# Kernel optimization log

Hardware: AMD Instinct MI355X
Metric: run time of the kernel (lower is better)

## Reference

```python
import jax, jax.numpy as jnp
import numpy as np

N = 50000
E = 800000
C_IN = 128
C_OUT = 128
HID = 2 * C_OUT


def setup_inputs() -> dict:
    key = jax.random.key(0)
    k1, k2, k3, k4, k5, k6, k7, k8 = jax.random.split(key, 8)
    node_feats = jax.random.normal(k1, (N, C_IN), dtype=jnp.float32)
    edge_index = jax.random.randint(k2, (2, E), 0, N, dtype=jnp.int64)
    edge_attr = jax.random.uniform(k3, (E,), dtype=jnp.float32)
    s1 = 1.0 / np.sqrt(C_IN)
    s2 = 1.0 / np.sqrt(HID)
    W1 = jax.random.uniform(k4, (C_IN, HID), dtype=jnp.float32, minval=-s1, maxval=s1)
    b1 = jax.random.uniform(k5, (HID,), dtype=jnp.float32, minval=-s1, maxval=s1)
    W2 = jax.random.uniform(k6, (HID, C_OUT), dtype=jnp.float32, minval=-s2, maxval=s2)
    b2 = jax.random.uniform(k7, (C_OUT,), dtype=jnp.float32, minval=-s2, maxval=s2)
    return {"node_feats": node_feats, "edge_index": edge_index, "edge_attr": edge_attr,
            "W1": W1, "b1": b1, "W2": W2, "b2": b2}


def _wl_conv_continuous(x, edge_index, edge_attr):
    # PyG WLConvContinuous: mean-aggregate weighted neighbor feats, then 0.5*(x + agg)
    src, dst = edge_index[0], edge_index[1]
    msg = x[src] * edge_attr[:, None]                      # [E, C_IN]
    agg = jax.ops.segment_sum(msg, dst, num_segments=N)    # [N, C_IN]
    deg = jax.ops.segment_sum(jnp.ones((E,), x.dtype), dst, num_segments=N)
    agg = agg / jnp.maximum(deg, 1.0)[:, None]             # mean aggregation
    return 0.5 * (x + agg)


def reference(node_feats, edge_index, edge_attr, W1, b1, W2, b2):
    out = _wl_conv_continuous(node_feats, edge_index, edge_attr)
    h = jax.nn.relu(out @ W1 + b1)
    return h @ W2 + b2
```

## Files before the change

kernel.cpp:

```cpp
#include <hip/hip_runtime.h>

#define C 128
#define HID 256
#define MT 64
#define EPB 2048
#define BSH 8
#define CAP 12288
#define OUTCAP (CAP + 2048)

typedef __attribute__((ext_vector_type(8))) short bf16x8;
typedef __attribute__((ext_vector_type(4))) short s16x4;
typedef __attribute__((ext_vector_type(4))) float f32x4;

__device__ inline unsigned short f2b(float f) {
    unsigned u = __builtin_bit_cast(unsigned, f);
    unsigned r = u + 0x7fffu + ((u >> 16) & 1u);
    return (unsigned short)(r >> 16);
}


__global__ __launch_bounds__(256) void fused_pre(
    const float* __restrict__ x, const float* __restrict__ W1,
    const float* __restrict__ W2, unsigned short* __restrict__ xb,
    unsigned short* __restrict__ W1p, unsigned short* __restrict__ W2p,
    int* __restrict__ cursor, long total4, int xblocks)
{
    const int bid = blockIdx.x;
    const int t = threadIdx.x;
    if (bid < xblocks) {
        long i = (long)bid * 256 + t;
        if (i < total4) {
            float4 v = *(const float4*)(x + i * 4);
            ushort4 o;
            o.x = f2b(v.x); o.y = f2b(v.y); o.z = f2b(v.z); o.w = f2b(v.w);
            *(ushort4*)(xb + i * 4) = o;
        }
    } else {
        if (bid == xblocks) cursor[t] = 0;
        int tt = (bid - xblocks) * 256 + t;
        if (tt < C * HID) {
            {
                int j = tt & 7, l = (tt >> 3) & 63, kk = (tt >> 9) & 3, nt = tt >> 11;
                int n = nt * 16 + (l & 15);
                int k = kk * 32 + 16 * (j >> 2) + 4 * (l >> 4) + (j & 3);
                W1p[tt] = f2b(W1[k * HID + n]);
            }
            {
                int j = tt & 7, l = (tt >> 3) & 63, kk = (tt >> 9) & 7, nt = tt >> 12;
                int n = nt * 16 + (l & 15);
                int k = kk * 32 + 16 * (j >> 2) + 4 * (l >> 4) + (j & 3);
                W2p[tt] = f2b(W2[k * C + n]);
            }
        }
    }
}


__global__ __launch_bounds__(256) void bucket_scatter(
    const int* __restrict__ ei, const float* __restrict__ ea,
    int* __restrict__ cursor, uint2* __restrict__ tmp, int E, int NB)
{
    __shared__ unsigned recx[EPB];
    __shared__ float    recw[EPB];
    __shared__ unsigned char bkt[EPB];
    __shared__ int bins[256];
    const int t = threadIdx.x;
    const int base = blockIdx.x * EPB;
    const int n = min(EPB, E - base);
    bins[t] = 0;
    __syncthreads();
    for (int i = t; i < n; i += 256) {
        int src = ei[base + i];
        int dst = ei[E + base + i];
        recx[i] = (unsigned)src | ((unsigned)(dst & 255) << 24);
        recw[i] = ea[base + i];
        int b = dst >> BSH;
        bkt[i] = (unsigned char)b;
        atomicAdd(&bins[b], 1);
    }
    __syncthreads();
    int myCount = bins[t];
    __syncthreads();
    int myBase = 0;
    if (t < NB && myCount > 0) myBase = atomicAdd(&cursor[t], myCount);
    bins[t] = t * CAP + myBase;
    __syncthreads();
    for (int i = t; i < n; i += 256) {
        int b = bkt[i];
        int pos = atomicAdd(&bins[b], 1);
        tmp[pos] = uint2{recx[i], __builtin_bit_cast(unsigned, recw[i])};
    }
}


__global__ __launch_bounds__(256) void bucket_sort(
    const uint2* __restrict__ tmp, const int* __restrict__ cursor,
    uint2* __restrict__ src_w, int* __restrict__ deg_i, int* __restrict__ offs,
    int N)
{
    __shared__ int cnt[256];
    __shared__ int sc[256];
    const int b = blockIdx.x;
    const int t = threadIdx.x;
    const int s0 = b * CAP;
    const int s1 = s0 + cursor[b];
    const int pbase = b * OUTCAP;
    cnt[t] = 0;
    __syncthreads();
    for (int i = s0 + t; i < s1; i += 256)
        atomicAdd(&cnt[tmp[i].x >> 24], 1);
    __syncthreads();
    const int d = cnt[t];
    const int pd = (d + 7) & ~7;
    sc[t] = pd;
    __syncthreads();
    for (int off = 1; off < 256; off <<= 1) {
        int v = (t >= off) ? sc[t - off] : 0;
        __syncthreads();
        sc[t] += v;
        __syncthreads();
    }
    const int my_off = pbase + sc[t] - pd;
    const int node = (b << BSH) + t;
    if (node < N) {
        deg_i[node] = d;
        offs[node]  = my_off;
    }
    cnt[t] = my_off;
    __syncthreads();
    for (int i = s0 + t; i < s1; i += 256) {
        uint2 r = tmp[i];
        int pos = atomicAdd(&cnt[r.x >> 24], 1);
        r.x &= 0x00ffffffu;
        src_w[pos] = r;
    }
    const uint2 zero{0u, 0u};
    for (int i = my_off + d; i < my_off + pd; ++i) src_w[i] = zero;
}


__global__ __launch_bounds__(512) void node_agg(
    const float* __restrict__ x, const unsigned short* __restrict__ xb,
    const int* __restrict__ offs, const int* __restrict__ deg_i,
    const uint2* __restrict__ src_w, unsigned short* __restrict__ out0, int N)
{
    const int lane = threadIdx.x & 63;
    const int wid  = threadIdx.x >> 6;
    const int node = blockIdx.x * 8 + wid;
    if (node >= N) return;
    const int rs = offs[node];
    const int d  = deg_i[node];
    const int pd = (d + 7) & ~7;
    const int c  = lane * 2;
    float a0 = 0.f, a1 = 0.f;
    int j = 0;
    for (; j + 16 <= pd; j += 16) {
        uint2 e[16];
        #pragma unroll
        for (int i = 0; i < 16; ++i) e[i] = src_w[rs + j + i];
        unsigned v[16];
        #pragma unroll
        for (int i = 0; i < 16; ++i)
            v[i] = *(const unsigned*)(xb + (long)e[i].x * C + c);
        #pragma unroll
        for (int i = 0; i < 16; ++i) {
            float w = __builtin_bit_cast(float, e[i].y);
            a0 = fmaf(__builtin_bit_cast(float, v[i] << 16), w, a0);
            a1 = fmaf(__builtin_bit_cast(float, v[i] & 0xffff0000u), w, a1);
        }
    }
    if (j < pd) {
        uint2 e[8];
        #pragma unroll
        for (int i = 0; i < 8; ++i) e[i] = src_w[rs + j + i];
        unsigned v[8];
        #pragma unroll
        for (int i = 0; i < 8; ++i)
            v[i] = *(const unsigned*)(xb + (long)e[i].x * C + c);
        #pragma unroll
        for (int i = 0; i < 8; ++i) {
            float w = __builtin_bit_cast(float, e[i].y);
            a0 = fmaf(__builtin_bit_cast(float, v[i] << 16), w, a0);
            a1 = fmaf(__builtin_bit_cast(float, v[i] & 0xffff0000u), w, a1);
        }
    }
    float dd  = (d > 0) ? (float)d : 1.f;
    float inv = 1.f / dd;
    float2 xv = *(const float2*)(x + (long)node * C + c);
    float o0 = 0.5f * (xv.x + a0 * inv);
    float o1 = 0.5f * (xv.y + a1 * inv);
    unsigned pack = (unsigned)f2b(o0) | ((unsigned)f2b(o1) << 16);
    *(unsigned*)(out0 + (long)node * C + c) = pack;
}


__global__ __launch_bounds__(256) void mlp_mfma(
    const unsigned short* __restrict__ out0,
    const unsigned short* __restrict__ W1p, const float* __restrict__ b1,
    const unsigned short* __restrict__ W2p, const float* __restrict__ b2,
    float* __restrict__ out, int N)
{
    __shared__ unsigned short hS[64][264];
    const int lane = threadIdx.x & 63;
    const int w    = threadIdx.x >> 6;
    const int r16  = lane & 15;
    const int grp  = lane >> 4;
    const int nodeBase = blockIdx.x * MT;

    bf16x8 bw1[4][4];
    #pragma unroll
    for (int n4 = 0; n4 < 4; ++n4)
        #pragma unroll
        for (int kk = 0; kk < 4; ++kk)
            bw1[n4][kk] = *(const bf16x8*)(W1p + ((((w * 4 + n4) * 4 + kk) * 64 + lane) << 3));

    #pragma unroll
    for (int rt = 0; rt < 4; ++rt) {
        int arow = nodeBase + rt * 16 + r16;
        if (arow >= N) arow = N - 1;
        const unsigned short* ar = out0 + (long)arow * C;
        bf16x8 a1[4];
        #pragma unroll
        for (int kk = 0; kk < 4; ++kk) {
            s16x4 lo = *(const s16x4*)(ar + kk * 32 + 4 * grp);
            s16x4 hi = *(const s16x4*)(ar + kk * 32 + 16 + 4 * grp);
            bf16x8 a;
            a[0] = lo[0]; a[1] = lo[1]; a[2] = lo[2]; a[3] = lo[3];
            a[4] = hi[0]; a[5] = hi[1]; a[6] = hi[2]; a[7] = hi[3];
            a1[kk] = a;
        }
        #pragma unroll
        for (int n4 = 0; n4 < 4; ++n4) {
            f32x4 acc = {0.f, 0.f, 0.f, 0.f};
            #pragma unroll
            for (int kk = 0; kk < 4; ++kk)
                acc = __builtin_amdgcn_mfma_f32_16x16x32_bf16(a1[kk], bw1[n4][kk], acc, 0, 0, 0);
            float bias = b1[(w * 4 + n4) * 16 + r16];
            #pragma unroll
            for (int r = 0; r < 4; ++r) {
                float h = fmaxf(acc[r] + bias, 0.f);
                hS[rt * 16 + grp * 4 + r][(w * 4 + n4) * 16 + r16] = f2b(h);
            }
        }
    }

    __syncthreads();

    bf16x8 bw2[2][8];
    #pragma unroll
    for (int n2 = 0; n2 < 2; ++n2)
        #pragma unroll
        for (int kk = 0; kk < 8; ++kk)
            bw2[n2][kk] = *(const bf16x8*)(W2p + ((((w * 2 + n2) * 8 + kk) * 64 + lane) << 3));

    #pragma unroll
    for (int rt = 0; rt < 4; ++rt) {
        bf16x8 a2[8];
        #pragma unroll
        for (int kk = 0; kk < 8; ++kk) {
            s16x4 lo = *(const s16x4*)&hS[rt * 16 + r16][kk * 32 + 4 * grp];
            s16x4 hi = *(const s16x4*)&hS[rt * 16 + r16][kk * 32 + 16 + 4 * grp];
            bf16x8 a;
            a[0] = lo[0]; a[1] = lo[1]; a[2] = lo[2]; a[3] = lo[3];
            a[4] = hi[0]; a[5] = hi[1]; a[6] = hi[2]; a[7] = hi[3];
            a2[kk] = a;
        }
        #pragma unroll
        for (int n2 = 0; n2 < 2; ++n2) {
            f32x4 acc = {0.f, 0.f, 0.f, 0.f};
            #pragma unroll
            for (int kk = 0; kk < 8; ++kk)
                acc = __builtin_amdgcn_mfma_f32_16x16x32_bf16(a2[kk], bw2[n2][kk], acc, 0, 0, 0);
            float bias = b2[(w * 2 + n2) * 16 + r16];
            #pragma unroll
            for (int r = 0; r < 4; ++r) {
                int node = nodeBase + rt * 16 + grp * 4 + r;
                if (node < N) out[(long)node * C + (w * 2 + n2) * 16 + r16] = acc[r] + bias;
            }
        }
    }
}

extern "C" void kernel_launch(void* const* d_in, const int* in_sizes, int n_in,
                              void* d_out, int out_size, void* d_ws, size_t ws_size,
                              hipStream_t stream) {
    const float* x  = (const float*)d_in[0];
    const int*   ei = (const int*)d_in[1];
    const float* ea = (const float*)d_in[2];
    const float* W1 = (const float*)d_in[3];
    const float* b1 = (const float*)d_in[4];
    const float* W2 = (const float*)d_in[5];
    const float* b2 = (const float*)d_in[6];
    float* out = (float*)d_out;
    const int N = in_sizes[0] / C;
    const int E = in_sizes[2];

    const int NB   = (N + 255) >> BSH;
    const int NBLK = (E + EPB - 1) / EPB;

    char* p = (char*)d_ws;
    auto alloc = [&](size_t bytes) { char* q = p; p += (bytes + 15) & ~(size_t)15; return q; };
    int* deg_i   = (int*)alloc((size_t)N * 4);
    int* offs    = (int*)alloc((size_t)N * 4);
    int* cursor  = (int*)alloc(256 * 4);
    uint2* src_w = (uint2*)alloc((size_t)NB * OUTCAP * 8);
    size_t tmp_bytes  = (size_t)NB * CAP * 8;
    size_t out0_bytes = (size_t)N * C * 2;
    char* out0_raw    = alloc(tmp_bytes > out0_bytes ? tmp_bytes : out0_bytes);
    unsigned short* out0 = (unsigned short*)out0_raw;
    uint2* tmp        = (uint2*)out0_raw;
    unsigned short* W1p = (unsigned short*)alloc((size_t)C * HID * 2);
    unsigned short* W2p = (unsigned short*)alloc((size_t)HID * C * 2);
    unsigned short* xb  = (unsigned short*)alloc((size_t)N * C * 2);

    const long total4 = ((long)N * C) / 4;
    const int xblocks = (int)((total4 + 255) / 256);
    const int wblocks = (C * HID + 255) / 256;

    fused_pre<<<xblocks + wblocks, 256, 0, stream>>>(
        x, W1, W2, xb, W1p, W2p, cursor, total4, xblocks);
    bucket_scatter<<<NBLK, 256, 0, stream>>>(ei, ea, cursor, tmp, E, NB);
    bucket_sort<<<NB, 256, 0, stream>>>(tmp, cursor, src_w, deg_i, offs, N);
    node_agg<<<(N + 7) / 8, 512, 0, stream>>>(x, xb, offs, deg_i, src_w, out0, N);
    mlp_mfma<<<(N + MT - 1) / MT, 256, 0, stream>>>(out0, W1p, b1, W2p, b2, out, N);
}
```

Measured before the change: 102.1 us.

## Fuse neighbor aggregation into MFMA MLP kernel via shared-memory tile

Merges the node aggregation and MLP kernels into one kernel of 512 threads per block. Eight waves each aggregate 8 nodes into a 64-row bf16 tile in LDS, and that tile then feeds the two MFMA GEMMs, which are now split across 8 waves instead of 4. This removes the global round trip of the intermediate bf16 activations and one kernel launch. The block size of the edge-scatter stage is also halved. In exchange, the MLP phase cannot start until the slowest node in the block finishes aggregating, and LDS use per block rises, which may limit occupancy.

```diff
diff --git a/kernel.cpp b/kernel.cpp
--- a/kernel.cpp
+++ b/kernel.cpp
@@ -2,8 +2,7 @@
 
 #define C 128
 #define HID 256
-#define MT 64
-#define EPB 2048
+#define EPB 1024
 #define BSH 8
 #define CAP 12288
 #define OUTCAP (CAP + 2048)
@@ -139,86 +138,84 @@
 }
 
 
-__global__ __launch_bounds__(512) void node_agg(
+__global__ __launch_bounds__(512, 6) void agg_mlp(
     const float* __restrict__ x, const unsigned short* __restrict__ xb,
     const int* __restrict__ offs, const int* __restrict__ deg_i,
-    const uint2* __restrict__ src_w, unsigned short* __restrict__ out0, int N)
-{
-    const int lane = threadIdx.x & 63;
-    const int wid  = threadIdx.x >> 6;
-    const int node = blockIdx.x * 8 + wid;
-    if (node >= N) return;
-    const int rs = offs[node];
-    const int d  = deg_i[node];
-    const int pd = (d + 7) & ~7;
-    const int c  = lane * 2;
-    float a0 = 0.f, a1 = 0.f;
-    int j = 0;
-    for (; j + 16 <= pd; j += 16) {
-        uint2 e[16];
-        #pragma unroll
-        for (int i = 0; i < 16; ++i) e[i] = src_w[rs + j + i];
-        unsigned v[16];
-        #pragma unroll
-        for (int i = 0; i < 16; ++i)
-            v[i] = *(const unsigned*)(xb + (long)e[i].x * C + c);
-        #pragma unroll
-        for (int i = 0; i < 16; ++i) {
-            float w = __builtin_bit_cast(float, e[i].y);
-            a0 = fmaf(__builtin_bit_cast(float, v[i] << 16), w, a0);
-            a1 = fmaf(__builtin_bit_cast(float, v[i] & 0xffff0000u), w, a1);
-        }
-    }
-    if (j < pd) {
-        uint2 e[8];
-        #pragma unroll
-        for (int i = 0; i < 8; ++i) e[i] = src_w[rs + j + i];
-        unsigned v[8];
-        #pragma unroll
-        for (int i = 0; i < 8; ++i)
-            v[i] = *(const unsigned*)(xb + (long)e[i].x * C + c);
-        #pragma unroll
-        for (int i = 0; i < 8; ++i) {
-            float w = __builtin_bit_cast(float, e[i].y);
-            a0 = fmaf(__builtin_bit_cast(float, v[i] << 16), w, a0);
-            a1 = fmaf(__builtin_bit_cast(float, v[i] & 0xffff0000u), w, a1);
-        }
-    }
-    float dd  = (d > 0) ? (float)d : 1.f;
-    float inv = 1.f / dd;
-    float2 xv = *(const float2*)(x + (long)node * C + c);
-    float o0 = 0.5f * (xv.x + a0 * inv);
-    float o1 = 0.5f * (xv.y + a1 * inv);
-    unsigned pack = (unsigned)f2b(o0) | ((unsigned)f2b(o1) << 16);
-    *(unsigned*)(out0 + (long)node * C + c) = pack;
-}
-
-
-__global__ __launch_bounds__(256) void mlp_mfma(
-    const unsigned short* __restrict__ out0,
+    const uint2* __restrict__ src_w,
     const unsigned short* __restrict__ W1p, const float* __restrict__ b1,
     const unsigned short* __restrict__ W2p, const float* __restrict__ b2,
     float* __restrict__ out, int N)
 {
+    __shared__ unsigned o0S[64][66];
     __shared__ unsigned short hS[64][264];
     const int lane = threadIdx.x & 63;
     const int w    = threadIdx.x >> 6;
-    const int r16  = lane & 15;
-    const int grp  = lane >> 4;
-    const int nodeBase = blockIdx.x * MT;
-
-    bf16x8 bw1[4][4];
+    const int nodeBase = blockIdx.x * 64;
+
+    for (int k = 0; k < 8; ++k) {
+        const int row  = w * 8 + k;
+        const int node = nodeBase + row;
+        unsigned pack = 0u;
+        if (node < N) {
+            const int rs = offs[node];
+            const int d  = deg_i[node];
+            const int pd = (d + 7) & ~7;
+            const int c  = lane * 2;
+            float a0 = 0.f, a1v = 0.f;
+            int j = 0;
+            for (; j + 16 <= pd; j += 16) {
+                uint2 e[16];
+                #pragma unroll
+                for (int i = 0; i < 16; ++i) e[i] = src_w[rs + j + i];
+                unsigned v[16];
+                #pragma unroll
+                for (int i = 0; i < 16; ++i)
+                    v[i] = *(const unsigned*)(xb + (long)e[i].x * C + c);
+                #pragma unroll
+                for (int i = 0; i < 16; ++i) {
+                    float wg = __builtin_bit_cast(float, e[i].y);
+                    a0  = fmaf(__builtin_bit_cast(float, v[i] << 16), wg, a0);
+                    a1v = fmaf(__builtin_bit_cast(float, v[i] & 0xffff0000u), wg, a1v);
+                }
+            }
+            if (j < pd) {
+                uint2 e[8];
+                #pragma unroll
+                for (int i = 0; i < 8; ++i) e[i] = src_w[rs + j + i];
+                unsigned v[8];
+                #pragma unroll
+                for (int i = 0; i < 8; ++i)
+                    v[i] = *(const unsigned*)(xb + (long)e[i].x * C + c);
+                #pragma unroll
+                for (int i = 0; i < 8; ++i) {
+                    float wg = __builtin_bit_cast(float, e[i].y);
+                    a0  = fmaf(__builtin_bit_cast(float, v[i] << 16), wg, a0);
+                    a1v = fmaf(__builtin_bit_cast(float, v[i] & 0xffff0000u), wg, a1v);
+                }
+            }
+            float inv = (d > 0) ? 1.f / (float)d : 1.f;
+            float2 xv = *(const float2*)(x + (long)node * C + c);
+            float o0 = 0.5f * (xv.x + a0 * inv);
+            float o1 = 0.5f * (xv.y + a1v * inv);
+            pack = (unsigned)f2b(o0) | ((unsigned)f2b(o1) << 16);
+        }
+        o0S[row][lane] = pack;
+    }
+    __syncthreads();
+
+    const int r16 = lane & 15;
+    const int grp = lane >> 4;
+
+    bf16x8 bw1[2][4];
     #pragma unroll
-    for (int n4 = 0; n4 < 4; ++n4)
+    for (int n = 0; n < 2; ++n)
         #pragma unroll
         for (int kk = 0; kk < 4; ++kk)
-            bw1[n4][kk] = *(const bf16x8*)(W1p + ((((w * 4 + n4) * 4 + kk) * 64 + lane) << 3));
+            bw1[n][kk] = *(const bf16x8*)(W1p + ((((w * 2 + n) * 4 + kk) * 64 + lane) << 3));
 
     #pragma unroll
     for (int rt = 0; rt < 4; ++rt) {
-        int arow = nodeBase + rt * 16 + r16;
-        if (arow >= N) arow = N - 1;
-        const unsigned short* ar = out0 + (long)arow * C;
+        const unsigned short* ar = (const unsigned short*)o0S[rt * 16 + r16];
         bf16x8 a1[4];
         #pragma unroll
         for (int kk = 0; kk < 4; ++kk) {
@@ -230,29 +227,28 @@
             a1[kk] = a;
         }
         #pragma unroll
-        for (int n4 = 0; n4 < 4; ++n4) {
+        for (int n = 0; n < 2; ++n) {
             f32x4 acc = {0.f, 0.f, 0.f, 0.f};
             #pragma unroll
             for (int kk = 0; kk < 4; ++kk)
-                acc = __builtin_amdgcn_mfma_f32_16x16x32_bf16(a1[kk], bw1[n4][kk], acc, 0, 0, 0);
-            float bias = b1[(w * 4 + n4) * 16 + r16];
+                acc = __builtin_amdgcn_mfma_f32_16x16x32_bf16(a1[kk], bw1[n][kk], acc, 0, 0, 0);
+            float bias = b1[(w * 2 + n) * 16 + r16];
             #pragma unroll
             for (int r = 0; r < 4; ++r) {
                 float h = fmaxf(acc[r] + bias, 0.f);
-                hS[rt * 16 + grp * 4 + r][(w * 4 + n4) * 16 + r16] = f2b(h);
-            }
-        }
-    }
-
-    __syncthreads();
-
-    bf16x8 bw2[2][8];
+                hS[rt * 16 + grp * 4 + r][(w * 2 + n) * 16 + r16] = f2b(h);
+            }
+        }
+    }
+
+    __syncthreads();
+
+    bf16x8 bw2[8];
     #pragma unroll
-    for (int n2 = 0; n2 < 2; ++n2)
-        #pragma unroll
-        for (int kk = 0; kk < 8; ++kk)
-            bw2[n2][kk] = *(const bf16x8*)(W2p + ((((w * 2 + n2) * 8 + kk) * 64 + lane) << 3));
-
+    for (int kk = 0; kk < 8; ++kk)
+        bw2[kk] = *(const bf16x8*)(W2p + (((w * 8 + kk) * 64 + lane) << 3));
+
+    const float bias2 = b2[w * 16 + r16];
     #pragma unroll
     for (int rt = 0; rt < 4; ++rt) {
         bf16x8 a2[8];
@@ -265,18 +261,14 @@
             a[4] = hi[0]; a[5] = hi[1]; a[6] = hi[2]; a[7] = hi[3];
             a2[kk] = a;
         }
-        #pragma unroll
-        for (int n2 = 0; n2 < 2; ++n2) {
-            f32x4 acc = {0.f, 0.f, 0.f, 0.f};
-            #pragma unroll
-            for (int kk = 0; kk < 8; ++kk)
-                acc = __builtin_amdgcn_mfma_f32_16x16x32_bf16(a2[kk], bw2[n2][kk], acc, 0, 0, 0);
-            float bias = b2[(w * 2 + n2) * 16 + r16];
-            #pragma unroll
-            for (int r = 0; r < 4; ++r) {
-                int node = nodeBase + rt * 16 + grp * 4 + r;
-                if (node < N) out[(long)node * C + (w * 2 + n2) * 16 + r16] = acc[r] + bias;
-            }
+        f32x4 acc = {0.f, 0.f, 0.f, 0.f};
+        #pragma unroll
+        for (int kk = 0; kk < 8; ++kk)
+            acc = __builtin_amdgcn_mfma_f32_16x16x32_bf16(a2[kk], bw2[kk], acc, 0, 0, 0);
+        #pragma unroll
+        for (int r = 0; r < 4; ++r) {
+            int node = nodeBase + rt * 16 + grp * 4 + r;
+            if (node < N) out[(long)node * C + w * 16 + r16] = acc[r] + bias2;
         }
     }
 }
@@ -304,11 +296,7 @@
     int* offs    = (int*)alloc((size_t)N * 4);
     int* cursor  = (int*)alloc(256 * 4);
     uint2* src_w = (uint2*)alloc((size_t)NB * OUTCAP * 8);
-    size_t tmp_bytes  = (size_t)NB * CAP * 8;
-    size_t out0_bytes = (size_t)N * C * 2;
-    char* out0_raw    = alloc(tmp_bytes > out0_bytes ? tmp_bytes : out0_bytes);
-    unsigned short* out0 = (unsigned short*)out0_raw;
-    uint2* tmp        = (uint2*)out0_raw;
+    uint2* tmp   = (uint2*)alloc((size_t)NB * CAP * 8);
     unsigned short* W1p = (unsigned short*)alloc((size_t)C * HID * 2);
     unsigned short* W2p = (unsigned short*)alloc((size_t)HID * C * 2);
     unsigned short* xb  = (unsigned short*)alloc((size_t)N * C * 2);
@@ -321,6 +309,6 @@
         x, W1, W2, xb, W1p, W2p, cursor, total4, xblocks);
     bucket_scatter<<<NBLK, 256, 0, stream>>>(ei, ea, cursor, tmp, E, NB);
     bucket_sort<<<NB, 256, 0, stream>>>(tmp, cursor, src_w, deg_i, offs, N);
-    node_agg<<<(N + 7) / 8, 512, 0, stream>>>(x, xb, offs, deg_i, src_w, out0, N);
-    mlp_mfma<<<(N + MT - 1) / MT, 256, 0, stream>>>(out0, W1p, b1, W2p, b2, out, N);
-}
+    agg_mlp<<<(N + 63) / 64, 512, 0, stream>>>(
+        x, xb, offs, deg_i, src_w, W1p, b1, W2p, b2, out, N);
+}
```

Result: slower. 104.8 us (+2.6%).

## Move x bf16 conversion into sort kernel and restructure MLP per-wave row tiles

Applied to the files above, without the earlier changes.

The fp32-to-bf16 conversion of node features moves out of the first kernel and into extra blocks of the bucket sort kernel. The sort launches only NB blocks, so the conversion can fill otherwise idle CUs while the small pre-kernel finishes sooner. The MLP kernel is also restructured so each wave owns 16 rows and loops over every output tile, streaming weight fragments from global/L2 instead of holding a per-wave slice of the weights in registers. This lowers register pressure and shrinks shared-memory use to per-wave buffers, at the cost of more repeated weight loads per block.

```diff
diff --git a/kernel.cpp b/kernel.cpp
--- a/kernel.cpp
+++ b/kernel.cpp
@@ -19,38 +19,27 @@
 }
 
 
-__global__ __launch_bounds__(256) void fused_pre(
-    const float* __restrict__ x, const float* __restrict__ W1,
-    const float* __restrict__ W2, unsigned short* __restrict__ xb,
+__global__ __launch_bounds__(256) void init_k(
+    const float* __restrict__ W1, const float* __restrict__ W2,
     unsigned short* __restrict__ W1p, unsigned short* __restrict__ W2p,
-    int* __restrict__ cursor, long total4, int xblocks)
+    int* __restrict__ cursor)
 {
     const int bid = blockIdx.x;
     const int t = threadIdx.x;
-    if (bid < xblocks) {
-        long i = (long)bid * 256 + t;
-        if (i < total4) {
-            float4 v = *(const float4*)(x + i * 4);
-            ushort4 o;
-            o.x = f2b(v.x); o.y = f2b(v.y); o.z = f2b(v.z); o.w = f2b(v.w);
-            *(ushort4*)(xb + i * 4) = o;
-        }
-    } else {
-        if (bid == xblocks) cursor[t] = 0;
-        int tt = (bid - xblocks) * 256 + t;
-        if (tt < C * HID) {
-            {
-                int j = tt & 7, l = (tt >> 3) & 63, kk = (tt >> 9) & 3, nt = tt >> 11;
-                int n = nt * 16 + (l & 15);
-                int k = kk * 32 + 16 * (j >> 2) + 4 * (l >> 4) + (j & 3);
-                W1p[tt] = f2b(W1[k * HID + n]);
-            }
-            {
-                int j = tt & 7, l = (tt >> 3) & 63, kk = (tt >> 9) & 7, nt = tt >> 12;
-                int n = nt * 16 + (l & 15);
-                int k = kk * 32 + 16 * (j >> 2) + 4 * (l >> 4) + (j & 3);
-                W2p[tt] = f2b(W2[k * C + n]);
-            }
+    if (bid == 0) cursor[t] = 0;
+    int tt = bid * 256 + t;
+    if (tt < C * HID) {
+        {
+            int j = tt & 7, l = (tt >> 3) & 63, kk = (tt >> 9) & 3, nt = tt >> 11;
+            int n = nt * 16 + (l & 15);
+            int k = kk * 32 + 16 * (j >> 2) + 4 * (l >> 4) + (j & 3);
+            W1p[tt] = f2b(W1[k * HID + n]);
+        }
+        {
+            int j = tt & 7, l = (tt >> 3) & 63, kk = (tt >> 9) & 7, nt = tt >> 12;
+            int n = nt * 16 + (l & 15);
+            int k = kk * 32 + 16 * (j >> 2) + 4 * (l >> 4) + (j & 3);
+            W2p[tt] = f2b(W2[k * C + n]);
         }
     }
 }
@@ -93,15 +82,26 @@
 }
 
 
-__global__ __launch_bounds__(256) void bucket_sort(
+__global__ __launch_bounds__(256) void sort_xconv(
     const uint2* __restrict__ tmp, const int* __restrict__ cursor,
     uint2* __restrict__ src_w, int* __restrict__ deg_i, int* __restrict__ offs,
-    int N)
-{
+    const float* __restrict__ x, unsigned short* __restrict__ xb,
+    long total4, int N, int NB)
+{
+    const int t = threadIdx.x;
+    if ((int)blockIdx.x >= NB) {
+        long i = (long)(blockIdx.x - NB) * 256 + t;
+        if (i < total4) {
+            float4 v = *(const float4*)(x + i * 4);
+            ushort4 o;
+            o.x = f2b(v.x); o.y = f2b(v.y); o.z = f2b(v.z); o.w = f2b(v.w);
+            *(ushort4*)(xb + i * 4) = o;
+        }
+        return;
+    }
     __shared__ int cnt[256];
     __shared__ int sc[256];
     const int b = blockIdx.x;
-    const int t = threadIdx.x;
     const int s0 = b * CAP;
     const int s1 = s0 + cursor[b];
     const int pbase = b * OUTCAP;
@@ -200,26 +200,18 @@
     const unsigned short* __restrict__ W2p, const float* __restrict__ b2,
     float* __restrict__ out, int N)
 {
-    __shared__ unsigned short hS[64][264];
+    __shared__ unsigned short hS[4][16][264];
     const int lane = threadIdx.x & 63;
-    const int w    = threadIdx.x >> 6;
+    const int wid  = threadIdx.x >> 6;
     const int r16  = lane & 15;
     const int grp  = lane >> 4;
-    const int nodeBase = blockIdx.x * MT;
-
-    bf16x8 bw1[4][4];
-    #pragma unroll
-    for (int n4 = 0; n4 < 4; ++n4)
-        #pragma unroll
-        for (int kk = 0; kk < 4; ++kk)
-            bw1[n4][kk] = *(const bf16x8*)(W1p + ((((w * 4 + n4) * 4 + kk) * 64 + lane) << 3));
-
-    #pragma unroll
-    for (int rt = 0; rt < 4; ++rt) {
-        int arow = nodeBase + rt * 16 + r16;
+    const int nodeBase = blockIdx.x * MT + wid * 16;
+
+    bf16x8 a1[4];
+    {
+        int arow = nodeBase + r16;
         if (arow >= N) arow = N - 1;
         const unsigned short* ar = out0 + (long)arow * C;
-        bf16x8 a1[4];
         #pragma unroll
         for (int kk = 0; kk < 4; ++kk) {
             s16x4 lo = *(const s16x4*)(ar + kk * 32 + 4 * grp);
@@ -229,54 +221,50 @@
             a[4] = hi[0]; a[5] = hi[1]; a[6] = hi[2]; a[7] = hi[3];
             a1[kk] = a;
         }
-        #pragma unroll
-        for (int n4 = 0; n4 < 4; ++n4) {
-            f32x4 acc = {0.f, 0.f, 0.f, 0.f};
-            #pragma unroll
-            for (int kk = 0; kk < 4; ++kk)
-                acc = __builtin_amdgcn_mfma_f32_16x16x32_bf16(a1[kk], bw1[n4][kk], acc, 0, 0, 0);
-            float bias = b1[(w * 4 + n4) * 16 + r16];
-            #pragma unroll
-            for (int r = 0; r < 4; ++r) {
-                float h = fmaxf(acc[r] + bias, 0.f);
-                hS[rt * 16 + grp * 4 + r][(w * 4 + n4) * 16 + r16] = f2b(h);
-            }
-        }
-    }
-
-    __syncthreads();
-
-    bf16x8 bw2[2][8];
+    }
+
+    #pragma unroll 4
+    for (int nt = 0; nt < 16; ++nt) {
+        f32x4 acc = {0.f, 0.f, 0.f, 0.f};
+        #pragma unroll
+        for (int kk = 0; kk < 4; ++kk) {
+            bf16x8 b = *(const bf16x8*)(W1p + (((nt * 4 + kk) * 64 + lane) << 3));
+            acc = __builtin_amdgcn_mfma_f32_16x16x32_bf16(a1[kk], b, acc, 0, 0, 0);
+        }
+        float bias = b1[nt * 16 + r16];
+        #pragma unroll
+        for (int r = 0; r < 4; ++r) {
+            float h = fmaxf(acc[r] + bias, 0.f);
+            hS[wid][grp * 4 + r][nt * 16 + r16] = f2b(h);
+        }
+    }
+
+    __syncthreads();
+
+    bf16x8 a2[8];
     #pragma unroll
-    for (int n2 = 0; n2 < 2; ++n2)
-        #pragma unroll
-        for (int kk = 0; kk < 8; ++kk)
-            bw2[n2][kk] = *(const bf16x8*)(W2p + ((((w * 2 + n2) * 8 + kk) * 64 + lane) << 3));
-
-    #pragma unroll
-    for (int rt = 0; rt < 4; ++rt) {
-        bf16x8 a2[8];
+    for (int kk = 0; kk < 8; ++kk) {
+        s16x4 lo = *(const s16x4*)&hS[wid][r16][kk * 32 + 4 * grp];
+        s16x4 hi = *(const s16x4*)&hS[wid][r16][kk * 32 + 16 + 4 * grp];
+        bf16x8 a;
+        a[0] = lo[0]; a[1] = lo[1]; a[2] = lo[2]; a[3] = lo[3];
+        a[4] = hi[0]; a[5] = hi[1]; a[6] = hi[2]; a[7] = hi[3];
+        a2[kk] = a;
+    }
+
+    #pragma unroll 2
+    for (int nt = 0; nt < 8; ++nt) {
+        f32x4 acc = {0.f, 0.f, 0.f, 0.f};
         #pragma unroll
         for (int kk = 0; kk < 8; ++kk) {
-            s16x4 lo = *(const s16x4*)&hS[rt * 16 + r16][kk * 32 + 4 * grp];
-            s16x4 hi = *(const s16x4*)&hS[rt * 16 + r16][kk * 32 + 16 + 4 * grp];
-            bf16x8 a;
-            a[0] = lo[0]; a[1] = lo[1]; a[2] = lo[2]; a[3] = lo[3];
-            a[4] = hi[0]; a[5] = hi[1]; a[6] = hi[2]; a[7] = hi[3];
-            a2[kk] = a;
-        }
-        #pragma unroll
-        for (int n2 = 0; n2 < 2; ++n2) {
-            f32x4 acc = {0.f, 0.f, 0.f, 0.f};
-            #pragma unroll
-            for (int kk = 0; kk < 8; ++kk)
-                acc = __builtin_amdgcn_mfma_f32_16x16x32_bf16(a2[kk], bw2[n2][kk], acc, 0, 0, 0);
-            float bias = b2[(w * 2 + n2) * 16 + r16];
-            #pragma unroll
-            for (int r = 0; r < 4; ++r) {
-                int node = nodeBase + rt * 16 + grp * 4 + r;
-                if (node < N) out[(long)node * C + (w * 2 + n2) * 16 + r16] = acc[r] + bias;
-            }
+            bf16x8 b = *(const bf16x8*)(W2p + (((nt * 8 + kk) * 64 + lane) << 3));
+            acc = __builtin_amdgcn_mfma_f32_16x16x32_bf16(a2[kk], b, acc, 0, 0, 0);
+        }
+        float bias = b2[nt * 16 + r16];
+        #pragma unroll
+        for (int r = 0; r < 4; ++r) {
+            int node = nodeBase + grp * 4 + r;
+            if (node < N) out[(long)node * C + nt * 16 + r16] = acc[r] + bias;
         }
     }
 }
@@ -317,10 +305,10 @@
     const int xblocks = (int)((total4 + 255) / 256);
     const int wblocks = (C * HID + 255) / 256;
 
-    fused_pre<<<xblocks + wblocks, 256, 0, stream>>>(
-        x, W1, W2, xb, W1p, W2p, cursor, total4, xblocks);
+    init_k<<<wblocks, 256, 0, stream>>>(W1, W2, W1p, W2p, cursor);
     bucket_scatter<<<NBLK, 256, 0, stream>>>(ei, ea, cursor, tmp, E, NB);
-    bucket_sort<<<NB, 256, 0, stream>>>(tmp, cursor, src_w, deg_i, offs, N);
+    sort_xconv<<<NB + xblocks, 256, 0, stream>>>(
+        tmp, cursor, src_w, deg_i, offs, x, xb, total4, N, NB);
     node_agg<<<(N + 7) / 8, 512, 0, stream>>>(x, xb, offs, deg_i, src_w, out0, N);
     mlp_mfma<<<(N + MT - 1) / MT, 256, 0, stream>>>(out0, W1p, b1, W2p, b2, out, N);
 }
```

After: 102.9 us. No clear change (+0.7%).
